# Kernel tuning notes

Hardware: AMD Instinct MI355X
Metric: run time of the kernel (lower is better)

Reference implementation:

```python
import jax, jax.numpy as jnp
import numpy as np

D_IN = 1024
D_OUT = 1024


def setup_inputs() -> dict:
    key = jax.random.key(0)
    k_x, k_q, k_k, k_v = jax.random.split(key, 4)
    x = jax.random.normal(k_x, (8, 2048, D_IN), dtype=jnp.float32)
    s = 1.0 / np.sqrt(D_IN)
    W_query = jax.random.uniform(k_q, (D_IN, D_OUT), jnp.float32, -s, s)
    W_key = jax.random.uniform(k_k, (D_IN, D_OUT), jnp.float32, -s, s)
    W_value = jax.random.uniform(k_v, (D_IN, D_OUT), jnp.float32, -s, s)
    return {"x": x, "W_query": W_query, "W_key": W_key, "W_value": W_value}


def reference(x, W_query, W_key, W_value):
    # x: [B, N, d_in]; weights stored as [d_in, d_out] (already transposed vs torch Linear)
    B, N, _ = x.shape
    q = x @ W_query          # [B, N, d_out]
    k = x @ W_key
    v = x @ W_value
    scores = jnp.einsum('bnd,bmd->bnm', q, k)  # [B, N, N]
    causal = jnp.tril(jnp.ones((N, N), dtype=bool))
    scores = jnp.where(causal, scores, -jnp.inf)
    weights = jax.nn.softmax(scores / np.sqrt(D_OUT), axis=-1)
    # dropout p=0.0 -> identity
    return jnp.einsum('bnm,bmd->bnd', weights, v)
```

## Files before the change

### kernel.cpp

```cpp
#include <hip/hip_runtime.h>
#include <hip/hip_bf16.h>

typedef unsigned short u16;
typedef unsigned int u32;
typedef __bf16 bf16x8 __attribute__((ext_vector_type(8)));
typedef float f32x4 __attribute__((ext_vector_type(4)));
typedef unsigned int u32x4 __attribute__((ext_vector_type(4)));

#define BATCH 8
#define SEQ   2048
#define DIM   1024
#define M_TOT (BATCH * SEQ)
#define N_QKV (3 * DIM)

#define OFF_QKV  ((size_t)0)
#define OFF_VT   ((size_t)100663296)
#define OFF_C    ((size_t)134217728)
#define OFF_XB   OFF_C
#define OFF_WT   (OFF_C + (size_t)33554432)
#define OFF_S    OFF_C

__device__ __forceinline__ u16 f32_to_bf16(float f) {
    u32 u = __builtin_bit_cast(u32, f);
    u = (u + 0x7fffu + ((u >> 16) & 1u)) >> 16;
    return (u16)u;
}

__device__ __forceinline__ float bf16_to_f32(u16 h) {
    u32 u = ((u32)h) << 16;
    return __builtin_bit_cast(float, u);
}

__device__ __forceinline__ bf16x8 lds_load8(const u16* p) {
    return __builtin_bit_cast(bf16x8, *(const u32x4*)p);
}

__device__ __forceinline__ void stage_tile(const u16* gA, size_t lda, u16* ldsA, int tid) {
    int wv = tid >> 6;
#pragma unroll
    for (int iss = 0; iss < 2; ++iss) {
        int c = iss * 256 + tid;
        int row = c >> 2;
        int kg = (c & 3) ^ ((c >> 3) & 3);
        const u16* gp = gA + (size_t)row * lda + (kg << 3);
        u16* lp = ldsA + (size_t)(iss * 256 + wv * 64) * 8;
        __builtin_amdgcn_global_load_lds((const __attribute__((address_space(1))) void*)gp,
                                         (__attribute__((address_space(3))) void*)lp,
                                         16, 0, 0);
    }
}

__device__ __forceinline__ void mfma_step(const u16* ldsA, const u16* ldsB, int tid,
                                          f32x4 acc[4][4]) {
    int lane = tid & 63;
    int wv = tid >> 6;
    int wr = (wv >> 1) * 64, wc = (wv & 1) * 64;
    int lrow = lane & 15, kg = lane >> 4;
    int skgA = ((kg ^ (((wr + lrow) >> 1) & 3)) << 3);
    int skgB = ((kg ^ (((wc + lrow) >> 1) & 3)) << 3);
    bf16x8 a[4], b[4];
#pragma unroll
    for (int i = 0; i < 4; ++i) {
        a[i] = lds_load8(&ldsA[(wr + i * 16 + lrow) * 32 + skgA]);
        b[i] = lds_load8(&ldsB[(wc + i * 16 + lrow) * 32 + skgB]);
    }
#pragma unroll
    for (int i = 0; i < 4; ++i)
#pragma unroll
        for (int j = 0; j < 4; ++j)
            acc[i][j] = __builtin_amdgcn_mfma_f32_16x16x32_bf16(a[i], b[j], acc[i][j], 0, 0, 0);
}

__global__ __launch_bounds__(256) void cast_x_kernel(const float* __restrict__ x,
                                                     u16* __restrict__ xb) {
    size_t g = (size_t)blockIdx.x * 256 + threadIdx.x;
    f32x4 v = ((const f32x4*)x)[g];
    u16 o[4] = {f32_to_bf16(v.x), f32_to_bf16(v.y), f32_to_bf16(v.z), f32_to_bf16(v.w)};
    *(unsigned long long*)(xb + g * 4) = *(const unsigned long long*)o;
}

__global__ __launch_bounds__(256) void transpose_w_kernel(const float* __restrict__ wq,
                                                          const float* __restrict__ wk,
                                                          const float* __restrict__ wv,
                                                          u16* __restrict__ wt) {
    __shared__ __align__(16) u16 tile[64][80];
    const float* w = blockIdx.z == 0 ? wq : (blockIdx.z == 1 ? wk : wv);
    int k0 = blockIdx.x * 64, n0 = blockIdx.y * 64;
    for (int g = threadIdx.x; g < 1024; g += 256) {
        int r = g >> 4, c = (g & 15) << 2;
        f32x4 v = *(const f32x4*)(w + (size_t)(k0 + r) * 1024 + n0 + c);
        tile[r][c + 0] = f32_to_bf16(v.x);
        tile[r][c + 1] = f32_to_bf16(v.y);
        tile[r][c + 2] = f32_to_bf16(v.z);
        tile[r][c + 3] = f32_to_bf16(v.w);
    }
    __syncthreads();
    u16* out = wt + (size_t)blockIdx.z * 1024 * 1024;
    for (int g = threadIdx.x; g < 512; g += 256) {
        int nr = g >> 3, kc = (g & 7) << 3;
        __align__(16) u16 tmp[8];
#pragma unroll
        for (int i = 0; i < 8; ++i) tmp[i] = tile[kc + i][nr];
        *(u32x4*)(out + (size_t)(n0 + nr) * 1024 + k0 + kc) = *(const u32x4*)tmp;
    }
}

__global__ __launch_bounds__(256, 2) void gemm_qkv_kernel(const u16* __restrict__ xb,
                                                          const u16* __restrict__ wt,
                                                          u16* __restrict__ qkv) {
    __shared__ __align__(16) u16 ldsA[128 * 32];
    __shared__ __align__(16) u16 ldsB[128 * 32];
    int nt = blockIdx.x, mt = blockIdx.y;
    const u16* A = xb + (size_t)mt * 128 * 1024;
    const u16* B = wt + (size_t)nt * 128 * 1024;
    int tid = threadIdx.x;
    f32x4 acc[4][4] = {};
    for (int kt = 0; kt < 32; ++kt) {
        __syncthreads();
        stage_tile(A + kt * 32, 1024, ldsA, tid);
        stage_tile(B + kt * 32, 1024, ldsB, tid);
        __syncthreads();
        mfma_step(ldsA, ldsB, tid, acc);
    }
    int lane = tid & 63, wv = tid >> 6;
    int wr = (wv >> 1) * 64, wc = (wv & 1) * 64;
    int r0 = (lane >> 4) * 4, c0 = lane & 15;
    size_t mbase = (size_t)mt * 128;
    int nbase = nt * 128;
#pragma unroll
    for (int i = 0; i < 4; ++i)
#pragma unroll
        for (int j = 0; j < 4; ++j) {
            int col = nbase + wc + j * 16 + c0;
            float scale = (col < 1024) ? 0.03125f : 1.0f;
#pragma unroll
            for (int r = 0; r < 4; ++r) {
                int row = wr + i * 16 + r0 + r;
                qkv[(mbase + row) * (size_t)N_QKV + col] = f32_to_bf16(acc[i][j][r] * scale);
            }
        }
}

__global__ __launch_bounds__(256) void transpose_v_kernel(const u16* __restrict__ qkv,
                                                          u16* __restrict__ vt) {
    __shared__ __align__(16) u16 tile[64][80];
    int m0 = blockIdx.x * 64, d0 = blockIdx.y * 64, b = blockIdx.z;
    const u16* src = qkv + (size_t)b * SEQ * N_QKV + 2048;
    for (int g = threadIdx.x; g < 512; g += 256) {
        int r = g >> 3, c = (g & 7) << 3;
        *(u32x4*)&tile[r][c] = *(const u32x4*)(src + (size_t)(m0 + r) * N_QKV + d0 + c);
    }
    __syncthreads();
    u16* dst = vt + (size_t)b * DIM * SEQ;
    for (int g = threadIdx.x; g < 512; g += 256) {
        int dr = g >> 3, mc = (g & 7) << 3;
        __align__(16) u16 tmp[8];
#pragma unroll
        for (int i = 0; i < 8; ++i) tmp[i] = tile[mc + i][dr];
        *(u32x4*)(dst + (size_t)(d0 + dr) * SEQ + m0 + mc) = *(const u32x4*)tmp;
    }
}

__global__ __launch_bounds__(256, 2) void gemm_scores_kernel(const u16* __restrict__ qkv,
                                                             u16* __restrict__ S) {
    int mtile = blockIdx.x, ntile = blockIdx.y, b = blockIdx.z;
    if (mtile > ntile) return;
    __shared__ __align__(16) u16 ldsA[128 * 32];
    __shared__ __align__(16) u16 ldsB[128 * 32];
    const u16* A = qkv + (size_t)b * SEQ * N_QKV + (size_t)ntile * 128 * N_QKV;
    const u16* B = qkv + (size_t)b * SEQ * N_QKV + (size_t)mtile * 128 * N_QKV + 1024;
    int tid = threadIdx.x;
    f32x4 acc[4][4] = {};
    for (int kt = 0; kt < 32; ++kt) {
        __syncthreads();
        stage_tile(A + kt * 32, N_QKV, ldsA, tid);
        stage_tile(B + kt * 32, N_QKV, ldsB, tid);
        __syncthreads();
        mfma_step(ldsA, ldsB, tid, acc);
    }
    u16* out = S + (size_t)b * SEQ * SEQ + (size_t)ntile * 128 * SEQ + (size_t)mtile * 128;
    int lane = tid & 63, wv = tid >> 6;
    int wr = (wv >> 1) * 64, wc = (wv & 1) * 64;
    int r0 = (lane >> 4) * 4, c0 = lane & 15;
#pragma unroll
    for (int i = 0; i < 4; ++i)
#pragma unroll
        for (int j = 0; j < 4; ++j) {
            int col = wc + j * 16 + c0;
#pragma unroll
            for (int r = 0; r < 4; ++r) {
                int row = wr + i * 16 + r0 + r;
                out[(size_t)row * SEQ + col] = f32_to_bf16(acc[i][j][r]);
            }
        }
}

__global__ __launch_bounds__(256) void softmax_kernel(u16* __restrict__ SP) {
    int gr = blockIdx.x;
    int b = gr >> 11, n = gr & 2047;
    u16* s = SP + ((size_t)b * SEQ + n) * SEQ;
    __shared__ float buf[2048];
    __shared__ float red[4];
    int t = threadIdx.x;
    int len = n + 1;
    float lmax = -3.0e38f;
    for (int m = t; m < len; m += 256) {
        float v = bf16_to_f32(s[m]);
        buf[m] = v;
        lmax = fmaxf(lmax, v);
    }
#pragma unroll
    for (int off = 32; off; off >>= 1) lmax = fmaxf(lmax, __shfl_xor(lmax, off, 64));
    if ((t & 63) == 0) red[t >> 6] = lmax;
    __syncthreads();
    float gmax = fmaxf(fmaxf(red[0], red[1]), fmaxf(red[2], red[3]));
    float lsum = 0.f;
    for (int m = t; m < len; m += 256) {
        float e = __expf(buf[m] - gmax);
        buf[m] = e;
        lsum += e;
    }
#pragma unroll
    for (int off = 32; off; off >>= 1) lsum += __shfl_xor(lsum, off, 64);
    __syncthreads();
    if ((t & 63) == 0) red[t >> 6] = lsum;
    __syncthreads();
    float inv = 1.0f / (red[0] + red[1] + red[2] + red[3]);
    for (int m = t; m < 2048; m += 256) {
        float v = (m < len) ? buf[m] * inv : 0.0f;
        s[m] = f32_to_bf16(v);
    }
}

__global__ __launch_bounds__(256, 2) void gemm_out_kernel(const u16* __restrict__ P,
                                                          const u16* __restrict__ vt,
                                                          float* __restrict__ O) {
    __shared__ __align__(16) u16 ldsA[128 * 32];
    __shared__ __align__(16) u16 ldsB[128 * 32];
    int dt = blockIdx.x, b = blockIdx.z;
    int ntile = (SEQ / 128 - 1) - blockIdx.y;
    const u16* A = P + (size_t)b * SEQ * SEQ + (size_t)ntile * 128 * SEQ;
    const u16* B = vt + (size_t)b * DIM * SEQ + (size_t)dt * 128 * SEQ;
    int tid = threadIdx.x;
    f32x4 acc[4][4] = {};
    int kTiles = ntile * 4 + 4;
    for (int kt = 0; kt < kTiles; ++kt) {
        __syncthreads();
        stage_tile(A + kt * 32, SEQ, ldsA, tid);
        stage_tile(B + kt * 32, SEQ, ldsB, tid);
        __syncthreads();
        mfma_step(ldsA, ldsB, tid, acc);
    }
    float* out = O + (size_t)b * SEQ * DIM + (size_t)ntile * 128 * DIM + (size_t)dt * 128;
    int lane = tid & 63, wv = tid >> 6;
    int wr = (wv >> 1) * 64, wc = (wv & 1) * 64;
    int r0 = (lane >> 4) * 4, c0 = lane & 15;
#pragma unroll
    for (int i = 0; i < 4; ++i)
#pragma unroll
        for (int j = 0; j < 4; ++j) {
            int col = wc + j * 16 + c0;
#pragma unroll
            for (int r = 0; r < 4; ++r) {
                int row = wr + i * 16 + r0 + r;
                out[(size_t)row * DIM + col] = acc[i][j][r];
            }
        }
}

extern "C" void kernel_launch(void* const* d_in, const int* in_sizes, int n_in,
                              void* d_out, int out_size, void* d_ws, size_t ws_size,
                              hipStream_t stream) {
    const float* x = (const float*)d_in[0];
    const float* wq = (const float*)d_in[1];
    const float* wk = (const float*)d_in[2];
    const float* wv = (const float*)d_in[3];
    char* ws = (char*)d_ws;
    u16* qkv = (u16*)(ws + OFF_QKV);
    u16* vt = (u16*)(ws + OFF_VT);
    u16* xb = (u16*)(ws + OFF_XB);
    u16* wt = (u16*)(ws + OFF_WT);
    u16* S = (u16*)(ws + OFF_S);
    float* O = (float*)d_out;

    cast_x_kernel<<<M_TOT * DIM / 4 / 256, 256, 0, stream>>>(x, xb);
    transpose_w_kernel<<<dim3(16, 16, 3), 256, 0, stream>>>(wq, wk, wv, wt);
    gemm_qkv_kernel<<<dim3(N_QKV / 128, M_TOT / 128), 256, 0, stream>>>(xb, wt, qkv);
    transpose_v_kernel<<<dim3(SEQ / 64, DIM / 64, BATCH), 256, 0, stream>>>(qkv, vt);
    gemm_scores_kernel<<<dim3(SEQ / 128, SEQ / 128, BATCH), 256, 0, stream>>>(qkv, S);
    softmax_kernel<<<BATCH * SEQ, 256, 0, stream>>>(S);
    gemm_out_kernel<<<dim3(DIM / 128, SEQ / 128, BATCH), 256, 0, stream>>>(S, vt, O);
}
```

Measured before the change: 448.9 us.

## Double GEMM K-tile depth, compact causal score grid, register-resident vectorized softmax

All three GEMMs now stage 64-wide K slices into LDS with an 8-way XOR swizzle, which halves the number of barrier-separated iterations and doubles the MFMAs done per sync. The scores GEMM launches only the 136 lower-triangular tiles per batch, decoding the tile indices with a sqrt, so empty blocks that returned early are no longer launched. Softmax keeps eight values per thread in registers and uses 16-byte vector loads and stores instead of a shared-memory buffer and scalar accesses. The cost is twice the LDS per block, which may reduce occupancy, plus a little index arithmetic per scores block.

New measurement: 398.7 us. 1.13x faster.

```diff
diff --git a/kernel.cpp b/kernel.cpp
--- a/kernel.cpp
+++ b/kernel.cpp
@@ -35,13 +35,13 @@
     return __builtin_bit_cast(bf16x8, *(const u32x4*)p);
 }
 
-__device__ __forceinline__ void stage_tile(const u16* gA, size_t lda, u16* ldsA, int tid) {
+__device__ __forceinline__ void stage_tile64(const u16* gA, size_t lda, u16* ldsA, int tid) {
     int wv = tid >> 6;
 #pragma unroll
-    for (int iss = 0; iss < 2; ++iss) {
-        int c = iss * 256 + tid;
-        int row = c >> 2;
-        int kg = (c & 3) ^ ((c >> 3) & 3);
+    for (int iss = 0; iss < 4; ++iss) {
+        int s = iss * 256 + tid;
+        int row = s >> 3;
+        int kg = (s & 7) ^ (row & 7);
         const u16* gp = gA + (size_t)row * lda + (kg << 3);
         u16* lp = ldsA + (size_t)(iss * 256 + wv * 64) * 8;
         __builtin_amdgcn_global_load_lds((const __attribute__((address_space(1))) void*)gp,
@@ -50,25 +50,28 @@
     }
 }
 
-__device__ __forceinline__ void mfma_step(const u16* ldsA, const u16* ldsB, int tid,
-                                          f32x4 acc[4][4]) {
+__device__ __forceinline__ void mfma_step64(const u16* ldsA, const u16* ldsB, int tid,
+                                            f32x4 acc[4][4]) {
     int lane = tid & 63;
     int wv = tid >> 6;
     int wr = (wv >> 1) * 64, wc = (wv & 1) * 64;
-    int lrow = lane & 15, kg = lane >> 4;
-    int skgA = ((kg ^ (((wr + lrow) >> 1) & 3)) << 3);
-    int skgB = ((kg ^ (((wc + lrow) >> 1) & 3)) << 3);
-    bf16x8 a[4], b[4];
-#pragma unroll
-    for (int i = 0; i < 4; ++i) {
-        a[i] = lds_load8(&ldsA[(wr + i * 16 + lrow) * 32 + skgA]);
-        b[i] = lds_load8(&ldsB[(wc + i * 16 + lrow) * 32 + skgB]);
-    }
-#pragma unroll
-    for (int i = 0; i < 4; ++i)
-#pragma unroll
-        for (int j = 0; j < 4; ++j)
-            acc[i][j] = __builtin_amdgcn_mfma_f32_16x16x32_bf16(a[i], b[j], acc[i][j], 0, 0, 0);
+    int lrow = lane & 15, kgl = lane >> 4;
+    int xr = lrow & 7;
+#pragma unroll
+    for (int ks = 0; ks < 2; ++ks) {
+        int off = ((ks * 4 + kgl) ^ xr) << 3;
+        bf16x8 a[4], b[4];
+#pragma unroll
+        for (int i = 0; i < 4; ++i) {
+            a[i] = lds_load8(&ldsA[(wr + i * 16 + lrow) * 64 + off]);
+            b[i] = lds_load8(&ldsB[(wc + i * 16 + lrow) * 64 + off]);
+        }
+#pragma unroll
+        for (int i = 0; i < 4; ++i)
+#pragma unroll
+            for (int j = 0; j < 4; ++j)
+                acc[i][j] = __builtin_amdgcn_mfma_f32_16x16x32_bf16(a[i], b[j], acc[i][j], 0, 0, 0);
+    }
 }
 
 __global__ __launch_bounds__(256) void cast_x_kernel(const float* __restrict__ x,
@@ -108,19 +111,19 @@
 __global__ __launch_bounds__(256, 2) void gemm_qkv_kernel(const u16* __restrict__ xb,
                                                           const u16* __restrict__ wt,
                                                           u16* __restrict__ qkv) {
-    __shared__ __align__(16) u16 ldsA[128 * 32];
-    __shared__ __align__(16) u16 ldsB[128 * 32];
+    __shared__ __align__(16) u16 ldsA[128 * 64];
+    __shared__ __align__(16) u16 ldsB[128 * 64];
     int nt = blockIdx.x, mt = blockIdx.y;
     const u16* A = xb + (size_t)mt * 128 * 1024;
     const u16* B = wt + (size_t)nt * 128 * 1024;
     int tid = threadIdx.x;
     f32x4 acc[4][4] = {};
-    for (int kt = 0; kt < 32; ++kt) {
-        __syncthreads();
-        stage_tile(A + kt * 32, 1024, ldsA, tid);
-        stage_tile(B + kt * 32, 1024, ldsB, tid);
-        __syncthreads();
-        mfma_step(ldsA, ldsB, tid, acc);
+    for (int kt = 0; kt < 16; ++kt) {
+        __syncthreads();
+        stage_tile64(A + kt * 64, 1024, ldsA, tid);
+        stage_tile64(B + kt * 64, 1024, ldsB, tid);
+        __syncthreads();
+        mfma_step64(ldsA, ldsB, tid, acc);
     }
     int lane = tid & 63, wv = tid >> 6;
     int wr = (wv >> 1) * 64, wc = (wv & 1) * 64;
@@ -163,20 +166,24 @@
 
 __global__ __launch_bounds__(256, 2) void gemm_scores_kernel(const u16* __restrict__ qkv,
                                                              u16* __restrict__ S) {
-    int mtile = blockIdx.x, ntile = blockIdx.y, b = blockIdx.z;
-    if (mtile > ntile) return;
-    __shared__ __align__(16) u16 ldsA[128 * 32];
-    __shared__ __align__(16) u16 ldsB[128 * 32];
+    int t = blockIdx.x;
+    int b = blockIdx.y;
+    int ntile = (int)((sqrtf(8.0f * (float)t + 1.0f) - 1.0f) * 0.5f);
+    while ((ntile + 1) * (ntile + 2) / 2 <= t) ++ntile;
+    while (ntile * (ntile + 1) / 2 > t) --ntile;
+    int mtile = t - ntile * (ntile + 1) / 2;
+    __shared__ __align__(16) u16 ldsA[128 * 64];
+    __shared__ __align__(16) u16 ldsB[128 * 64];
     const u16* A = qkv + (size_t)b * SEQ * N_QKV + (size_t)ntile * 128 * N_QKV;
     const u16* B = qkv + (size_t)b * SEQ * N_QKV + (size_t)mtile * 128 * N_QKV + 1024;
     int tid = threadIdx.x;
     f32x4 acc[4][4] = {};
-    for (int kt = 0; kt < 32; ++kt) {
-        __syncthreads();
-        stage_tile(A + kt * 32, N_QKV, ldsA, tid);
-        stage_tile(B + kt * 32, N_QKV, ldsB, tid);
-        __syncthreads();
-        mfma_step(ldsA, ldsB, tid, acc);
+    for (int kt = 0; kt < 16; ++kt) {
+        __syncthreads();
+        stage_tile64(A + kt * 64, N_QKV, ldsA, tid);
+        stage_tile64(B + kt * 64, N_QKV, ldsB, tid);
+        __syncthreads();
+        mfma_step64(ldsA, ldsB, tid, acc);
     }
     u16* out = S + (size_t)b * SEQ * SEQ + (size_t)ntile * 128 * SEQ + (size_t)mtile * 128;
     int lane = tid & 63, wv = tid >> 6;
@@ -197,59 +204,68 @@
 
 __global__ __launch_bounds__(256) void softmax_kernel(u16* __restrict__ SP) {
     int gr = blockIdx.x;
-    int b = gr >> 11, n = gr & 2047;
-    u16* s = SP + ((size_t)b * SEQ + n) * SEQ;
-    __shared__ float buf[2048];
+    int n = gr & 2047;
+    u16* s = SP + (size_t)gr * SEQ;
     __shared__ float red[4];
     int t = threadIdx.x;
+    int base = t << 3;
     int len = n + 1;
+    float v[8];
     float lmax = -3.0e38f;
-    for (int m = t; m < len; m += 256) {
-        float v = bf16_to_f32(s[m]);
-        buf[m] = v;
-        lmax = fmaxf(lmax, v);
+    if (base < len) {
+        u32x4 raw = *(const u32x4*)(s + base);
+        const u16* h = (const u16*)&raw;
+#pragma unroll
+        for (int i = 0; i < 8; ++i) {
+            v[i] = (base + i < len) ? bf16_to_f32(h[i]) : -3.0e38f;
+            lmax = fmaxf(lmax, v[i]);
+        }
+    } else {
+#pragma unroll
+        for (int i = 0; i < 8; ++i) v[i] = -3.0e38f;
     }
 #pragma unroll
     for (int off = 32; off; off >>= 1) lmax = fmaxf(lmax, __shfl_xor(lmax, off, 64));
     if ((t & 63) == 0) red[t >> 6] = lmax;
     __syncthreads();
     float gmax = fmaxf(fmaxf(red[0], red[1]), fmaxf(red[2], red[3]));
+    __syncthreads();
     float lsum = 0.f;
-    for (int m = t; m < len; m += 256) {
-        float e = __expf(buf[m] - gmax);
-        buf[m] = e;
+#pragma unroll
+    for (int i = 0; i < 8; ++i) {
+        float e = __expf(v[i] - gmax);
+        v[i] = e;
         lsum += e;
     }
 #pragma unroll
     for (int off = 32; off; off >>= 1) lsum += __shfl_xor(lsum, off, 64);
-    __syncthreads();
     if ((t & 63) == 0) red[t >> 6] = lsum;
     __syncthreads();
     float inv = 1.0f / (red[0] + red[1] + red[2] + red[3]);
-    for (int m = t; m < 2048; m += 256) {
-        float v = (m < len) ? buf[m] * inv : 0.0f;
-        s[m] = f32_to_bf16(v);
-    }
+    __align__(16) u16 o[8];
+#pragma unroll
+    for (int i = 0; i < 8; ++i) o[i] = f32_to_bf16(v[i] * inv);
+    *(u32x4*)(s + base) = *(const u32x4*)o;
 }
 
 __global__ __launch_bounds__(256, 2) void gemm_out_kernel(const u16* __restrict__ P,
                                                           const u16* __restrict__ vt,
                                                           float* __restrict__ O) {
-    __shared__ __align__(16) u16 ldsA[128 * 32];
-    __shared__ __align__(16) u16 ldsB[128 * 32];
+    __shared__ __align__(16) u16 ldsA[128 * 64];
+    __shared__ __align__(16) u16 ldsB[128 * 64];
     int dt = blockIdx.x, b = blockIdx.z;
     int ntile = (SEQ / 128 - 1) - blockIdx.y;
     const u16* A = P + (size_t)b * SEQ * SEQ + (size_t)ntile * 128 * SEQ;
     const u16* B = vt + (size_t)b * DIM * SEQ + (size_t)dt * 128 * SEQ;
     int tid = threadIdx.x;
     f32x4 acc[4][4] = {};
-    int kTiles = ntile * 4 + 4;
+    int kTiles = ntile * 2 + 2;
     for (int kt = 0; kt < kTiles; ++kt) {
         __syncthreads();
-        stage_tile(A + kt * 32, SEQ, ldsA, tid);
-        stage_tile(B + kt * 32, SEQ, ldsB, tid);
-        __syncthreads();
-        mfma_step(ldsA, ldsB, tid, acc);
+        stage_tile64(A + kt * 64, SEQ, ldsA, tid);
+        stage_tile64(B + kt * 64, SEQ, ldsB, tid);
+        __syncthreads();
+        mfma_step64(ldsA, ldsB, tid, acc);
     }
     float* out = O + (size_t)b * SEQ * DIM + (size_t)ntile * 128 * DIM + (size_t)dt * 128;
     int lane = tid & 63, wv = tid >> 6;
@@ -287,7 +303,7 @@
     transpose_w_kernel<<<dim3(16, 16, 3), 256, 0, stream>>>(wq, wk, wv, wt);
     gemm_qkv_kernel<<<dim3(N_QKV / 128, M_TOT / 128), 256, 0, stream>>>(xb, wt, qkv);
     transpose_v_kernel<<<dim3(SEQ / 64, DIM / 64, BATCH), 256, 0, stream>>>(qkv, vt);
-    gemm_scores_kernel<<<dim3(SEQ / 128, SEQ / 128, BATCH), 256, 0, stream>>>(qkv, S);
+    gemm_scores_kernel<<<dim3(136, BATCH), 256, 0, stream>>>(qkv, S);
     softmax_kernel<<<BATCH * SEQ, 256, 0, stream>>>(S);
     gemm_out_kernel<<<dim3(DIM / 128, SEQ / 128, BATCH), 256, 0, stream>>>(S, vt, O);
 }
```
